# Optimization experiments

Measured on AMD Instinct MI355X. Metric: run time of the kernel, lower is better.

## Reference

```python
import math
import jax, jax.numpy as jnp
import numpy as np

SEQ, BATCH, HID, N_HEAD = 1024, 8, 1024, 16


def setup_inputs() -> dict:
    key0 = jax.random.key(0)
    ks = jax.random.split(key0, 7)
    shp = (SEQ, BATCH, HID)
    w = lambda k: jax.random.normal(k, (HID, HID), dtype=jnp.float32) * 0.02
    return {
        "value": jax.random.normal(ks[0], shp, dtype=jnp.float32),
        "key": jax.random.normal(ks[1], shp, dtype=jnp.float32),
        "query": jax.random.normal(ks[2], shp, dtype=jnp.float32),
        "Wq": w(ks[3]), "Wk": w(ks[4]), "Wv": w(ks[5]), "Wo": w(ks[6]),
    }


def _proj_split(x, W, n_head, d_k):
    # x: (S,B,H) -> linear -> split heads -> stack heads along batch dim: (S, n_head*B, d_k)
    S, B, H = x.shape
    p = x @ W.T                                   # (S,B,H)
    p = p.reshape(S, B, n_head, d_k)
    p = p.transpose(0, 2, 1, 3).reshape(S, n_head * B, d_k)
    return p


def reference(value, key, query, Wq, Wk, Wv, Wo):
    S, B, H = value.shape
    n_head = N_HEAD
    d_k = H // n_head
    Q = _proj_split(query, Wq, n_head, d_k)       # (S, n_head*B, d_k)
    K = _proj_split(key, Wk, n_head, d_k)
    V = _proj_split(value, Wv, n_head, d_k)
    # scores[b,i,j] = K_i . Q_j / sqrt(d_k)  (note: rows = key index, cols = query index)
    scores = jnp.einsum('ibd,jbd->bij', K, Q) / math.sqrt(d_k)  # (n_head*B, S, S)
    future_mask = jnp.triu(jnp.ones((S, S), dtype=bool), 1)      # True where j > i
    scores = jnp.where(future_mask[None, :, :], -jnp.inf, scores)
    # faithful to original: softmax over dim=2 (the QUERY axis)
    dist = jax.nn.softmax(scores, axis=2)                         # (n_head*B, S, S)
    # att[j,b,d] = sum_i dist[b,i,j] * V[i,b,d]
    att = jnp.einsum('bij,ibd->jbd', dist, V)                     # (S, n_head*B, d_k)
    # un-stack heads: (S, n_head, B, d_k) -> (B, S, n_head*d_k)
    att = att.reshape(S, n_head, B, d_k).transpose(2, 0, 1, 3).reshape(B, S, H)
    out = (att @ Wo.T).transpose(1, 0, 2)                         # (S, B, H)
    return out, dist
```

## Files before the change

kernel.cpp:

```cpp
#include <hip/hip_runtime.h>
#include <hip/hip_bf16.h>
#include <stdint.h>

#define SQ   1024
#define NB   8
#define HD   1024
#define NHD  16
#define DKK  64

typedef __bf16 bf16x8_t __attribute__((ext_vector_type(8)));
typedef __bf16 bf16x4_t __attribute__((ext_vector_type(4)));
typedef float  f32x4_t  __attribute__((ext_vector_type(4)));
typedef __hip_bfloat16 bf16;

__device__ __forceinline__ void gld_lds16(const void* g, void* l) {
    __builtin_amdgcn_global_load_lds(
        (__attribute__((address_space(1))) void*)const_cast<void*>(g),
        (__attribute__((address_space(3))) void*)l,
        16, 0, 0);
}

__device__ __forceinline__ bf16x8_t cvt8(float4 a, float4 b) {
    bf16x8_t r;
    r[0] = (__bf16)a.x; r[1] = (__bf16)a.y; r[2] = (__bf16)a.z; r[3] = (__bf16)a.w;
    r[4] = (__bf16)b.x; r[5] = (__bf16)b.y; r[6] = (__bf16)b.z; r[7] = (__bf16)b.w;
    return r;
}

__device__ __forceinline__ void stage64(const char* gbase, int rowstride,
                                        char* lbase, int w, int lane) {
#pragma unroll
    for (int q = 0; q < 2; ++q) {
        const int cid = (q * 4 + w) * 64 + lane;
        const int r   = cid >> 3;
        const int cc  = (cid & 7) ^ ((r ^ (r >> 3)) & 7);
        gld_lds16(gbase + r * rowstride + cc * 16, lbase + cid * 16);
    }
}

__global__ __launch_bounds__(256, 2)
void gemm_kernel(const void* __restrict__ A0, const void* __restrict__ A1,
                 const void* __restrict__ A2,
                 const float* __restrict__ W0, const float* __restrict__ W1,
                 const float* __restrict__ W2,
                 void* __restrict__ O0, void* __restrict__ O1,
                 void* __restrict__ O2, int mode)
{
    const int z = blockIdx.z;
    const void*  A  = (z == 0) ? A0 : (z == 1) ? A1 : A2;
    const float* Wf = (z == 0) ? W0 : (z == 1) ? W1 : W2;
    void*        Ov = (z == 0) ? O0 : (z == 1) ? O1 : O2;

    __shared__ alignas(16) bf16 lA[2][128 * 32];
    __shared__ alignas(16) bf16 lB[2][128 * 32];

    const int tid  = threadIdx.x;
    const int lane = tid & 63;
    const int w    = tid >> 6;
    const int wr   = w >> 1;
    const int wc   = w & 1;
    const int g    = lane >> 4;
    const int ln   = lane & 15;
    const int bm   = blockIdx.y;
    const int bn   = blockIdx.x;

    f32x4_t acc[4][4];
#pragma unroll
    for (int i = 0; i < 4; ++i)
#pragma unroll
        for (int j = 0; j < 4; ++j)
            acc[i][j] = (f32x4_t){0.f, 0.f, 0.f, 0.f};

    const size_t arow0 = (size_t)bm * 128;
    const size_t brow0 = (size_t)bn * 128;
    const float* Af = (const float*)A;
    const bf16*  Ab = (const bf16*)A;

    int scid[2], srow[2], sch[2];
#pragma unroll
    for (int q = 0; q < 2; ++q) {
        const int cid = (q * 4 + w) * 64 + lane;
        scid[q] = cid;
        srow[q] = cid >> 2;
        sch[q]  = (cid & 3) ^ ((srow[q] ^ (srow[q] >> 2)) & 3);
    }

    float4 pa[4], pw[4];

    auto issue_loads = [&](int k0, int buf) {
#pragma unroll
        for (int q = 0; q < 2; ++q) {
            const float4* wsrc = (const float4*)(Wf + (brow0 + srow[q]) * HD + k0 + sch[q] * 8);
            pw[q * 2]     = wsrc[0];
            pw[q * 2 + 1] = wsrc[1];
        }
        if (mode == 0) {
#pragma unroll
            for (int q = 0; q < 2; ++q) {
                const float4* asrc = (const float4*)(Af + (arow0 + srow[q]) * HD + k0 + sch[q] * 8);
                pa[q * 2]     = asrc[0];
                pa[q * 2 + 1] = asrc[1];
            }
        } else {
#pragma unroll
            for (int q = 0; q < 2; ++q)
                gld_lds16((const char*)Ab + ((arow0 + srow[q]) * HD + k0) * 2 + sch[q] * 16,
                          (char*)&lA[buf][0] + scid[q] * 16);
        }
    };
    auto commit_writes = [&](int buf) {
#pragma unroll
        for (int q = 0; q < 2; ++q)
            *(bf16x8_t*)&lB[buf][scid[q] * 8] = cvt8(pw[q * 2], pw[q * 2 + 1]);
        if (mode == 0) {
#pragma unroll
            for (int q = 0; q < 2; ++q)
                *(bf16x8_t*)&lA[buf][scid[q] * 8] = cvt8(pa[q * 2], pa[q * 2 + 1]);
        }
    };

    issue_loads(0, 0);
    commit_writes(0);
    __syncthreads();

    int cur = 0;
    for (int ks = 0; ks < 32; ++ks) {
        if (ks < 31) issue_loads((ks + 1) * 32, cur ^ 1);
        bf16x8_t av[4], bv[4];
#pragma unroll
        for (int mi = 0; mi < 4; ++mi) {
            const int row = wr * 64 + mi * 16 + ln;
            av[mi] = *(const bf16x8_t*)&lA[cur][row * 32 + ((g ^ ((row ^ (row >> 2)) & 3)) << 3)];
        }
#pragma unroll
        for (int ni = 0; ni < 4; ++ni) {
            const int row = wc * 64 + ni * 16 + ln;
            bv[ni] = *(const bf16x8_t*)&lB[cur][row * 32 + ((g ^ ((row ^ (row >> 2)) & 3)) << 3)];
        }
#pragma unroll
        for (int mi = 0; mi < 4; ++mi)
#pragma unroll
            for (int ni = 0; ni < 4; ++ni)
                acc[mi][ni] = __builtin_amdgcn_mfma_f32_16x16x32_bf16(
                    av[mi], bv[ni], acc[mi][ni], 0, 0, 0);
        if (ks < 31) commit_writes(cur ^ 1);
        __syncthreads();
        cur ^= 1;
    }

    bf16*  Ob = (bf16*)Ov;
    float* Of = (float*)Ov;
#pragma unroll
    for (int mi = 0; mi < 4; ++mi) {
#pragma unroll
        for (int ni = 0; ni < 4; ++ni) {
            const int o = bn * 128 + wc * 64 + ni * 16 + ln;
#pragma unroll
            for (int r = 0; r < 4; ++r) {
                const int m = bm * 128 + wr * 64 + mi * 16 + g * 4 + r;
                const float v = acc[mi][ni][r];
                if (mode == 0) {
                    const int h = o >> 6, d = o & 63;
                    const int s = m >> 3, b = m & 7;
                    if (z == 2)
                        Ob[((size_t)((h * 8 + b) * DKK + d)) * SQ + s] = __float2bfloat16(v);
                    else
                        Ob[(((size_t)(h * 8 + b) * SQ + s) << 6) + d] = __float2bfloat16(v);
                } else {
                    Of[(size_t)m * HD + o] = v;
                }
            }
        }
    }
}

__global__ __launch_bounds__(256, 2)
void rowsum_kernel(const bf16* __restrict__ Kh, const bf16* __restrict__ Qh,
                   float* __restrict__ invS)
{
    __shared__ alignas(16) bf16 Kl[64 * 64];
    __shared__ alignas(16) bf16 Ql[2][64 * 64];
    const int tid = threadIdx.x, lane = tid & 63, w = tid >> 6;
    const int g = lane >> 4, ln = lane & 15;
    const int ib = 15 - (int)blockIdx.x, bh = blockIdx.y;
    const char* Kp = (const char*)(Kh + ((size_t)bh * SQ + ib * 64) * DKK);
    const char* Qp = (const char*)(Qh + (size_t)bh * SQ * DKK);

    stage64(Kp, 128, (char*)Kl, w, lane);
    stage64(Qp, 128, (char*)Ql[0], w, lane);
    __syncthreads();

    const int arow = w * 16 + ln;
    const int asw  = (arow ^ (arow >> 3)) & 7;
    const bf16x8_t ak0 = *(const bf16x8_t*)&Kl[arow * 64 + ((g ^ asw) << 3)];
    const bf16x8_t ak1 = *(const bf16x8_t*)&Kl[arow * 64 + (((4 + g) ^ asw) << 3)];
    const int irow = ib * 64 + w * 16 + g * 4;

    float lsum[4] = {0.f, 0.f, 0.f, 0.f};
    int cur = 0;
    for (int jt = 0; jt <= ib; ++jt) {
        if (jt < ib)
            stage64(Qp + (size_t)(jt + 1) * 8192, 128, (char*)Ql[cur ^ 1], w, lane);
#pragma unroll
        for (int nf = 0; nf < 4; ++nf) {
            const int brow = nf * 16 + ln;
            const int bsw  = (brow ^ (brow >> 3)) & 7;
            bf16x8_t b0 = *(const bf16x8_t*)&Ql[cur][brow * 64 + ((g ^ bsw) << 3)];
            bf16x8_t b1 = *(const bf16x8_t*)&Ql[cur][brow * 64 + (((4 + g) ^ bsw) << 3)];
            f32x4_t a = (f32x4_t){0.f, 0.f, 0.f, 0.f};
            __builtin_amdgcn_s_setprio(1);
            a = __builtin_amdgcn_mfma_f32_16x16x32_bf16(ak0, b0, a, 0, 0, 0);
            a = __builtin_amdgcn_mfma_f32_16x16x32_bf16(ak1, b1, a, 0, 0, 0);
            __builtin_amdgcn_s_setprio(0);
            const int j = jt * 64 + nf * 16 + ln;
#pragma unroll
            for (int r = 0; r < 4; ++r)
                lsum[r] += (j <= irow + r) ? __expf(a[r] * 0.125f) : 0.f;
        }
        __syncthreads();
        cur ^= 1;
    }
#pragma unroll
    for (int r = 0; r < 4; ++r) {
        float p = lsum[r];
        p += __shfl_xor(p, 1);
        p += __shfl_xor(p, 2);
        p += __shfl_xor(p, 4);
        p += __shfl_xor(p, 8);
        lsum[r] = p;
    }
    if (ln == 0) {
#pragma unroll
        for (int r = 0; r < 4; ++r)
            invS[(size_t)bh * SQ + irow + r] = 1.f / lsum[r];
    }
}

__global__ __launch_bounds__(256, 2)
void dist_pv_kernel(const bf16* __restrict__ Kh, const bf16* __restrict__ Qh,
                    const bf16* __restrict__ Vt, const float* __restrict__ invS,
                    float* __restrict__ Dist, bf16* __restrict__ att4)
{
    __shared__ alignas(16) bf16 Kl[2][64 * 64];
    __shared__ alignas(16) bf16 Vl[2][64 * 64];
    __shared__ alignas(16) bf16 Ql[64 * 64];
    __shared__ alignas(16) bf16 dT[64 * 72];
    __shared__ alignas(16) float dF[64 * 68];
    const int tid = threadIdx.x, lane = tid & 63, w = tid >> 6;
    const int g = lane >> 4, ln = lane & 15;
    const int jb = blockIdx.x, bh = blockIdx.y;
    const char* Kp = (const char*)(Kh + (size_t)bh * SQ * DKK);
    const char* Qp = (const char*)(Qh + (size_t)bh * SQ * DKK);
    const char* Vp = (const char*)(Vt + (size_t)bh * DKK * SQ);
    float* Dp = Dist + (size_t)bh * SQ * SQ;
    const float* ivp = invS + (size_t)bh * SQ;

    stage64(Qp + (size_t)jb * 8192, 128, (char*)Ql, w, lane);
    __syncthreads();
    bf16x8_t bq[4][2];
#pragma unroll
    for (int nf = 0; nf < 4; ++nf) {
        const int brow = nf * 16 + ln;
        const int bsw  = (brow ^ (brow >> 3)) & 7;
        bq[nf][0] = *(const bf16x8_t*)&Ql[brow * 64 + ((g ^ bsw) << 3)];
        bq[nf][1] = *(const bf16x8_t*)&Ql[brow * 64 + (((4 + g) ^ bsw) << 3)];
    }

    stage64(Kp + (size_t)jb * 8192, 128, (char*)Kl[0], w, lane);
    stage64(Vp + (size_t)jb * 128, 2048, (char*)Vl[0], w, lane);

    const f32x4_t zero4 = (f32x4_t){0.f, 0.f, 0.f, 0.f};
    for (int it0 = 0; it0 < jb; ++it0) {
#pragma unroll
        for (int q = 0; q < 4; ++q) {
            const int cid = q * 256 + tid;
            const int row = cid >> 4, ch = cid & 15;
            *(f32x4_t*)(Dp + (size_t)(it0 * 64 + row) * SQ + jb * 64 + ch * 4) = zero4;
        }
    }
    __syncthreads();

    const int arow = w * 16 + ln;
    const int asw  = (arow ^ (arow >> 3)) & 7;
    f32x4_t accPV[4];
#pragma unroll
    for (int nf = 0; nf < 4; ++nf) accPV[nf] = zero4;

    int cur = 0;
    for (int it = jb; it < 16; ++it) {
        if (it < 15) {
            stage64(Kp + (size_t)(it + 1) * 8192, 128, (char*)Kl[cur ^ 1], w, lane);
            stage64(Vp + (size_t)(it + 1) * 128, 2048, (char*)Vl[cur ^ 1], w, lane);
        }
        const int i0 = it * 64 + w * 16 + g * 4;
        float iv[4];
#pragma unroll
        for (int r = 0; r < 4; ++r) iv[r] = ivp[i0 + r];

        const bf16x8_t ak0 = *(const bf16x8_t*)&Kl[cur][arow * 64 + ((g ^ asw) << 3)];
        const bf16x8_t ak1 = *(const bf16x8_t*)&Kl[cur][arow * 64 + (((4 + g) ^ asw) << 3)];
#pragma unroll
        for (int nf = 0; nf < 4; ++nf) {
            f32x4_t a = zero4;
            __builtin_amdgcn_s_setprio(1);
            a = __builtin_amdgcn_mfma_f32_16x16x32_bf16(ak0, bq[nf][0], a, 0, 0, 0);
            a = __builtin_amdgcn_mfma_f32_16x16x32_bf16(ak1, bq[nf][1], a, 0, 0, 0);
            __builtin_amdgcn_s_setprio(0);
            const int jl = nf * 16 + ln;
            const int j  = jb * 64 + jl;
            bf16x4_t pk;
#pragma unroll
            for (int r = 0; r < 4; ++r) {
                const float e = (j <= i0 + r) ? __expf(a[r] * 0.125f) * iv[r] : 0.f;
                dF[(w * 16 + g * 4 + r) * 68 + jl] = e;
                pk[r] = (__bf16)e;
            }
            *(bf16x4_t*)&dT[jl * 72 + ((w * 16 + g * 4) ^ (((jl >> 3) & 7) << 3))] = pk;
        }
        __syncthreads();

#pragma unroll
        for (int q = 0; q < 4; ++q) {
            const int cid = q * 256 + tid;
            const int row = cid >> 4;
            const int jc  = (cid & 15) << 2;
            const f32x4_t fv = *(const f32x4_t*)&dF[row * 68 + jc];
            *(f32x4_t*)(Dp + (size_t)(it * 64 + row) * SQ + jb * 64 + jc) = fv;
        }
#pragma unroll
        for (int kk = 0; kk < 2; ++kk) {
            const int abase = (kk * 32 + g * 8) ^ (((arow >> 3) & 7) << 3);
            const bf16x8_t a = *(const bf16x8_t*)&dT[arow * 72 + abase];
            __builtin_amdgcn_s_setprio(1);
#pragma unroll
            for (int nf = 0; nf < 4; ++nf) {
                const int brow = nf * 16 + ln;
                const int bsw  = (brow ^ (brow >> 3)) & 7;
                const bf16x8_t b =
                    *(const bf16x8_t*)&Vl[cur][brow * 64 + (((kk * 4 + g) ^ bsw) << 3)];
                accPV[nf] = __builtin_amdgcn_mfma_f32_16x16x32_bf16(a, b, accPV[nf], 0, 0, 0);
            }
            __builtin_amdgcn_s_setprio(0);
        }
        __syncthreads();
        cur ^= 1;
    }

    const int h = bh >> 3, b = bh & 7;
#pragma unroll
    for (int nf = 0; nf < 4; ++nf) {
#pragma unroll
        for (int r = 0; r < 4; ++r) {
            const int j = jb * 64 + w * 16 + g * 4 + r;
            att4[(size_t)(j * 8 + b) * HD + h * 64 + nf * 16 + ln] =
                __float2bfloat16(accPV[nf][r]);
        }
    }
}

extern "C" void kernel_launch(void* const* d_in, const int* in_sizes, int n_in,
                              void* d_out, int out_size, void* d_ws, size_t ws_size,
                              hipStream_t stream)
{
    const float* value = (const float*)d_in[0];
    const float* key_  = (const float*)d_in[1];
    const float* query = (const float*)d_in[2];
    const float* Wq    = (const float*)d_in[3];
    const float* Wk    = (const float*)d_in[4];
    const float* Wv    = (const float*)d_in[5];
    const float* Wo    = (const float*)d_in[6];

    float* out  = (float*)d_out;
    float* dist = out + (size_t)SQ * NB * HD;
    float* invS = out;

    char* ws   = (char*)d_ws;
    bf16* Qh   = (bf16*)(ws);
    bf16* Kh   = (bf16*)(ws + (size_t)16 * 1024 * 1024);
    bf16* Vt   = (bf16*)(ws + (size_t)32 * 1024 * 1024);
    bf16* att4 = (bf16*)(ws + (size_t)48 * 1024 * 1024);

    dim3 blk(256);
    gemm_kernel<<<dim3(8, 64, 3), blk, 0, stream>>>(
        query, key_, value, Wq, Wk, Wv, Qh, Kh, Vt, 0);
    rowsum_kernel<<<dim3(16, 128), blk, 0, stream>>>(Kh, Qh, invS);
    dist_pv_kernel<<<dim3(16, 128), blk, 0, stream>>>(Kh, Qh, Vt, invS, dist, att4);
    gemm_kernel<<<dim3(8, 64, 1), blk, 0, stream>>>(
        att4, att4, att4, Wo, Wo, Wo, out, out, out, 1);
}
```

Measured before the change: 940.8 us.

## Pre-convert inputs to bf16, triple-buffer projection GEMM, restructure dist/PV pipeline

Adds a separate conversion pass that turns the fp32 activations and weights into bf16 scratch held in the dist output region, so the QKV projection GEMM can stage both operands through direct global-to-LDS loads with a 3-stage buffer and explicit vmcnt waits. Upper-triangle zeroing of dist moves from the dist/PV kernel into the rowsum kernel. The dist/PV kernel drops its fp32 LDS staging tile and writes probabilities straight to global, and uses double-buffered dT with lighter barriers. Occupancy hints are raised. The trade is an extra conversion pass over the inputs in exchange for less in-loop conversion and fewer barriers, at the risk of less coalesced dist stores.

```diff
diff --git a/kernel.cpp b/kernel.cpp
--- a/kernel.cpp
+++ b/kernel.cpp
@@ -13,6 +13,8 @@
 typedef float  f32x4_t  __attribute__((ext_vector_type(4)));
 typedef __hip_bfloat16 bf16;
 
+#define SB0() __builtin_amdgcn_sched_barrier(0)
+
 __device__ __forceinline__ void gld_lds16(const void* g, void* l) {
     __builtin_amdgcn_global_load_lds(
         (__attribute__((address_space(1))) void*)const_cast<void*>(g),
@@ -20,6 +22,19 @@
         16, 0, 0);
 }
 
+__device__ __forceinline__ void vm_bar() {
+    SB0();
+    asm volatile("s_waitcnt vmcnt(0) lgkmcnt(0)" ::: "memory");
+    __builtin_amdgcn_s_barrier();
+    SB0();
+}
+__device__ __forceinline__ void lgkm_bar() {
+    SB0();
+    asm volatile("s_waitcnt lgkmcnt(0)" ::: "memory");
+    __builtin_amdgcn_s_barrier();
+    SB0();
+}
+
 __device__ __forceinline__ bf16x8_t cvt8(float4 a, float4 b) {
     bf16x8_t r;
     r[0] = (__bf16)a.x; r[1] = (__bf16)a.y; r[2] = (__bf16)a.z; r[3] = (__bf16)a.w;
@@ -38,21 +53,47 @@
     }
 }
 
-__global__ __launch_bounds__(256, 2)
-void gemm_kernel(const void* __restrict__ A0, const void* __restrict__ A1,
-                 const void* __restrict__ A2,
-                 const float* __restrict__ W0, const float* __restrict__ W1,
-                 const float* __restrict__ W2,
-                 void* __restrict__ O0, void* __restrict__ O1,
-                 void* __restrict__ O2, int mode)
+__device__ __forceinline__ void stage_g(const char* gbase, char* lbase,
+                                        int w, int lane) {
+#pragma unroll
+    for (int q = 0; q < 2; ++q) {
+        const int cid = (q * 4 + w) * 64 + lane;
+        const int r   = cid >> 2;
+        const int ch  = (cid & 3) ^ ((r ^ (r >> 2)) & 3);
+        gld_lds16(gbase + r * (HD * 2) + ch * 16, lbase + cid * 16);
+    }
+}
+
+__global__ __launch_bounds__(256)
+void cvt_kernel(const float* __restrict__ s0, const float* __restrict__ s1,
+                const float* __restrict__ s2,
+                bf16* __restrict__ d0, bf16* __restrict__ d1,
+                bf16* __restrict__ d2)
 {
     const int z = blockIdx.z;
-    const void*  A  = (z == 0) ? A0 : (z == 1) ? A1 : A2;
-    const float* Wf = (z == 0) ? W0 : (z == 1) ? W1 : W2;
-    void*        Ov = (z == 0) ? O0 : (z == 1) ? O1 : O2;
-
-    __shared__ alignas(16) bf16 lA[2][128 * 32];
-    __shared__ alignas(16) bf16 lB[2][128 * 32];
+    const float* s = (z == 0) ? s0 : (z == 1) ? s1 : s2;
+    bf16*        d = (z == 0) ? d0 : (z == 1) ? d1 : d2;
+    const size_t i = ((size_t)blockIdx.x * 256 + threadIdx.x) * 8;
+    const float4 a = *(const float4*)(s + i);
+    const float4 b = *(const float4*)(s + i + 4);
+    *(bf16x8_t*)(d + i) = cvt8(a, b);
+}
+
+__global__ __launch_bounds__(256, 3)
+void gemm_bb(const bf16* __restrict__ A0, const bf16* __restrict__ A1,
+             const bf16* __restrict__ A2,
+             const bf16* __restrict__ B0, const bf16* __restrict__ B1,
+             const bf16* __restrict__ B2,
+             bf16* __restrict__ O0, bf16* __restrict__ O1,
+             bf16* __restrict__ O2)
+{
+    const int z = blockIdx.z;
+    const bf16* A  = (z == 0) ? A0 : (z == 1) ? A1 : A2;
+    const bf16* Bw = (z == 0) ? B0 : (z == 1) ? B1 : B2;
+    bf16*       Ob = (z == 0) ? O0 : (z == 1) ? O1 : O2;
+
+    __shared__ alignas(16) bf16 lA[3][128 * 32];
+    __shared__ alignas(16) bf16 lB[3][128 * 32];
 
     const int tid  = threadIdx.x;
     const int lane = tid & 63;
@@ -71,10 +112,93 @@
         for (int j = 0; j < 4; ++j)
             acc[i][j] = (f32x4_t){0.f, 0.f, 0.f, 0.f};
 
+    const char* Ap = (const char*)(A  + (size_t)bm * 128 * HD);
+    const char* Bp = (const char*)(Bw + (size_t)bn * 128 * HD);
+
+    auto stg = [&](int ks, int buf) {
+        stage_g(Ap + ks * 64, (char*)&lA[buf][0], w, lane);
+        stage_g(Bp + ks * 64, (char*)&lB[buf][0], w, lane);
+    };
+
+    stg(0, 0);
+    stg(1, 1);
+
+    for (int ks = 0; ks < 32; ++ks) {
+        const int buf = ks % 3;
+        SB0();
+        if (ks < 31) asm volatile("s_waitcnt vmcnt(4)" ::: "memory");
+        else         asm volatile("s_waitcnt vmcnt(0)" ::: "memory");
+        __builtin_amdgcn_s_barrier();
+        SB0();
+        if (ks < 30) stg(ks + 2, (ks + 2) % 3);
+
+        bf16x8_t av[4], bv[4];
+#pragma unroll
+        for (int mi = 0; mi < 4; ++mi) {
+            const int row = wr * 64 + mi * 16 + ln;
+            av[mi] = *(const bf16x8_t*)&lA[buf][row * 32 + ((g ^ ((row ^ (row >> 2)) & 3)) << 3)];
+        }
+#pragma unroll
+        for (int ni = 0; ni < 4; ++ni) {
+            const int row = wc * 64 + ni * 16 + ln;
+            bv[ni] = *(const bf16x8_t*)&lB[buf][row * 32 + ((g ^ ((row ^ (row >> 2)) & 3)) << 3)];
+        }
+        __builtin_amdgcn_s_setprio(1);
+#pragma unroll
+        for (int mi = 0; mi < 4; ++mi)
+#pragma unroll
+            for (int ni = 0; ni < 4; ++ni)
+                acc[mi][ni] = __builtin_amdgcn_mfma_f32_16x16x32_bf16(
+                    av[mi], bv[ni], acc[mi][ni], 0, 0, 0);
+        __builtin_amdgcn_s_setprio(0);
+    }
+
+#pragma unroll
+    for (int mi = 0; mi < 4; ++mi) {
+#pragma unroll
+        for (int ni = 0; ni < 4; ++ni) {
+            const int o = bn * 128 + wc * 64 + ni * 16 + ln;
+#pragma unroll
+            for (int r = 0; r < 4; ++r) {
+                const int m = bm * 128 + wr * 64 + mi * 16 + g * 4 + r;
+                const float v = acc[mi][ni][r];
+                const int h = o >> 6, d = o & 63;
+                const int s = m >> 3, b = m & 7;
+                if (z == 2)
+                    Ob[((size_t)((h * 8 + b) * DKK + d)) * SQ + s] = __float2bfloat16(v);
+                else
+                    Ob[(((size_t)(h * 8 + b) * SQ + s) << 6) + d] = __float2bfloat16(v);
+            }
+        }
+    }
+}
+
+__global__ __launch_bounds__(256, 2)
+void gemm_k4(const bf16* __restrict__ A, const float* __restrict__ Wf,
+             float* __restrict__ Of)
+{
+    __shared__ alignas(16) bf16 lA[2][128 * 32];
+    __shared__ alignas(16) bf16 lB[2][128 * 32];
+
+    const int tid  = threadIdx.x;
+    const int lane = tid & 63;
+    const int w    = tid >> 6;
+    const int wr   = w >> 1;
+    const int wc   = w & 1;
+    const int g    = lane >> 4;
+    const int ln   = lane & 15;
+    const int bm   = blockIdx.y;
+    const int bn   = blockIdx.x;
+
+    f32x4_t acc[4][4];
+#pragma unroll
+    for (int i = 0; i < 4; ++i)
+#pragma unroll
+        for (int j = 0; j < 4; ++j)
+            acc[i][j] = (f32x4_t){0.f, 0.f, 0.f, 0.f};
+
     const size_t arow0 = (size_t)bm * 128;
     const size_t brow0 = (size_t)bn * 128;
-    const float* Af = (const float*)A;
-    const bf16*  Ab = (const bf16*)A;
 
     int scid[2], srow[2], sch[2];
 #pragma unroll
@@ -85,7 +209,7 @@
         sch[q]  = (cid & 3) ^ ((srow[q] ^ (srow[q] >> 2)) & 3);
     }
 
-    float4 pa[4], pw[4];
+    float4 pw[4];
 
     auto issue_loads = [&](int k0, int buf) {
 #pragma unroll
@@ -94,29 +218,15 @@
             pw[q * 2]     = wsrc[0];
             pw[q * 2 + 1] = wsrc[1];
         }
-        if (mode == 0) {
-#pragma unroll
-            for (int q = 0; q < 2; ++q) {
-                const float4* asrc = (const float4*)(Af + (arow0 + srow[q]) * HD + k0 + sch[q] * 8);
-                pa[q * 2]     = asrc[0];
-                pa[q * 2 + 1] = asrc[1];
-            }
-        } else {
-#pragma unroll
-            for (int q = 0; q < 2; ++q)
-                gld_lds16((const char*)Ab + ((arow0 + srow[q]) * HD + k0) * 2 + sch[q] * 16,
-                          (char*)&lA[buf][0] + scid[q] * 16);
-        }
+#pragma unroll
+        for (int q = 0; q < 2; ++q)
+            gld_lds16((const char*)A + ((arow0 + srow[q]) * HD + k0) * 2 + sch[q] * 16,
+                      (char*)&lA[buf][0] + scid[q] * 16);
     };
     auto commit_writes = [&](int buf) {
 #pragma unroll
         for (int q = 0; q < 2; ++q)
             *(bf16x8_t*)&lB[buf][scid[q] * 8] = cvt8(pw[q * 2], pw[q * 2 + 1]);
-        if (mode == 0) {
-#pragma unroll
-            for (int q = 0; q < 2; ++q)
-                *(bf16x8_t*)&lA[buf][scid[q] * 8] = cvt8(pa[q * 2], pa[q * 2 + 1]);
-        }
     };
 
     issue_loads(0, 0);
@@ -148,8 +258,6 @@
         cur ^= 1;
     }
 
-    bf16*  Ob = (bf16*)Ov;
-    float* Of = (float*)Ov;
 #pragma unroll
     for (int mi = 0; mi < 4; ++mi) {
 #pragma unroll
@@ -158,25 +266,15 @@
 #pragma unroll
             for (int r = 0; r < 4; ++r) {
                 const int m = bm * 128 + wr * 64 + mi * 16 + g * 4 + r;
-                const float v = acc[mi][ni][r];
-                if (mode == 0) {
-                    const int h = o >> 6, d = o & 63;
-                    const int s = m >> 3, b = m & 7;
-                    if (z == 2)
-                        Ob[((size_t)((h * 8 + b) * DKK + d)) * SQ + s] = __float2bfloat16(v);
-                    else
-                        Ob[(((size_t)(h * 8 + b) * SQ + s) << 6) + d] = __float2bfloat16(v);
-                } else {
-                    Of[(size_t)m * HD + o] = v;
-                }
+                Of[(size_t)m * HD + o] = acc[mi][ni][r];
             }
         }
     }
 }
 
-__global__ __launch_bounds__(256, 2)
+__global__ __launch_bounds__(256, 4)
 void rowsum_kernel(const bf16* __restrict__ Kh, const bf16* __restrict__ Qh,
-                   float* __restrict__ invS)
+                   float* __restrict__ invS, float* __restrict__ Dist)
 {
     __shared__ alignas(16) bf16 Kl[64 * 64];
     __shared__ alignas(16) bf16 Ql[2][64 * 64];
@@ -185,10 +283,11 @@
     const int ib = 15 - (int)blockIdx.x, bh = blockIdx.y;
     const char* Kp = (const char*)(Kh + ((size_t)bh * SQ + ib * 64) * DKK);
     const char* Qp = (const char*)(Qh + (size_t)bh * SQ * DKK);
+    float* Dp = Dist + (size_t)bh * SQ * SQ;
 
     stage64(Kp, 128, (char*)Kl, w, lane);
     stage64(Qp, 128, (char*)Ql[0], w, lane);
-    __syncthreads();
+    vm_bar();
 
     const int arow = w * 16 + ln;
     const int asw  = (arow ^ (arow >> 3)) & 7;
@@ -197,16 +296,17 @@
     const int irow = ib * 64 + w * 16 + g * 4;
 
     float lsum[4] = {0.f, 0.f, 0.f, 0.f};
-    int cur = 0;
     for (int jt = 0; jt <= ib; ++jt) {
+        const int buf = jt & 1;
+        if (jt > 0) vm_bar();
         if (jt < ib)
-            stage64(Qp + (size_t)(jt + 1) * 8192, 128, (char*)Ql[cur ^ 1], w, lane);
+            stage64(Qp + (size_t)(jt + 1) * 8192, 128, (char*)Ql[buf ^ 1], w, lane);
 #pragma unroll
         for (int nf = 0; nf < 4; ++nf) {
             const int brow = nf * 16 + ln;
             const int bsw  = (brow ^ (brow >> 3)) & 7;
-            bf16x8_t b0 = *(const bf16x8_t*)&Ql[cur][brow * 64 + ((g ^ bsw) << 3)];
-            bf16x8_t b1 = *(const bf16x8_t*)&Ql[cur][brow * 64 + (((4 + g) ^ bsw) << 3)];
+            bf16x8_t b0 = *(const bf16x8_t*)&Ql[buf][brow * 64 + ((g ^ bsw) << 3)];
+            bf16x8_t b1 = *(const bf16x8_t*)&Ql[buf][brow * 64 + (((4 + g) ^ bsw) << 3)];
             f32x4_t a = (f32x4_t){0.f, 0.f, 0.f, 0.f};
             __builtin_amdgcn_s_setprio(1);
             a = __builtin_amdgcn_mfma_f32_16x16x32_bf16(ak0, b0, a, 0, 0, 0);
@@ -217,8 +317,6 @@
             for (int r = 0; r < 4; ++r)
                 lsum[r] += (j <= irow + r) ? __expf(a[r] * 0.125f) : 0.f;
         }
-        __syncthreads();
-        cur ^= 1;
     }
 #pragma unroll
     for (int r = 0; r < 4; ++r) {
@@ -234,18 +332,25 @@
         for (int r = 0; r < 4; ++r)
             invS[(size_t)bh * SQ + irow + r] = 1.f / lsum[r];
     }
-}
-
-__global__ __launch_bounds__(256, 2)
+    const f32x4_t zero4 = (f32x4_t){0.f, 0.f, 0.f, 0.f};
+    for (int jt = ib + 1; jt < 16; ++jt) {
+#pragma unroll
+        for (int q = 0; q < 4; ++q) {
+            const int cid = q * 256 + tid;
+            const int row = cid >> 4, ch = cid & 15;
+            *(f32x4_t*)(Dp + (size_t)(ib * 64 + row) * SQ + jt * 64 + ch * 4) = zero4;
+        }
+    }
+}
+
+__global__ __launch_bounds__(256, 3)
 void dist_pv_kernel(const bf16* __restrict__ Kh, const bf16* __restrict__ Qh,
                     const bf16* __restrict__ Vt, const float* __restrict__ invS,
                     float* __restrict__ Dist, bf16* __restrict__ att4)
 {
     __shared__ alignas(16) bf16 Kl[2][64 * 64];
     __shared__ alignas(16) bf16 Vl[2][64 * 64];
-    __shared__ alignas(16) bf16 Ql[64 * 64];
-    __shared__ alignas(16) bf16 dT[64 * 72];
-    __shared__ alignas(16) float dF[64 * 68];
+    __shared__ alignas(16) bf16 dT[2][64 * 72];
     const int tid = threadIdx.x, lane = tid & 63, w = tid >> 6;
     const int g = lane >> 4, ln = lane & 15;
     const int jb = blockIdx.x, bh = blockIdx.y;
@@ -255,53 +360,46 @@
     float* Dp = Dist + (size_t)bh * SQ * SQ;
     const float* ivp = invS + (size_t)bh * SQ;
 
-    stage64(Qp + (size_t)jb * 8192, 128, (char*)Ql, w, lane);
-    __syncthreads();
+    stage64(Qp + (size_t)jb * 8192, 128, (char*)&dT[0][0], w, lane);
+    stage64(Kp + (size_t)jb * 8192, 128, (char*)&Kl[0][0], w, lane);
+    stage64(Vp + (size_t)jb * 128, 2048, (char*)&Vl[0][0], w, lane);
+    vm_bar();
+
     bf16x8_t bq[4][2];
-#pragma unroll
-    for (int nf = 0; nf < 4; ++nf) {
-        const int brow = nf * 16 + ln;
-        const int bsw  = (brow ^ (brow >> 3)) & 7;
-        bq[nf][0] = *(const bf16x8_t*)&Ql[brow * 64 + ((g ^ bsw) << 3)];
-        bq[nf][1] = *(const bf16x8_t*)&Ql[brow * 64 + (((4 + g) ^ bsw) << 3)];
-    }
-
-    stage64(Kp + (size_t)jb * 8192, 128, (char*)Kl[0], w, lane);
-    stage64(Vp + (size_t)jb * 128, 2048, (char*)Vl[0], w, lane);
-
-    const f32x4_t zero4 = (f32x4_t){0.f, 0.f, 0.f, 0.f};
-    for (int it0 = 0; it0 < jb; ++it0) {
-#pragma unroll
-        for (int q = 0; q < 4; ++q) {
-            const int cid = q * 256 + tid;
-            const int row = cid >> 4, ch = cid & 15;
-            *(f32x4_t*)(Dp + (size_t)(it0 * 64 + row) * SQ + jb * 64 + ch * 4) = zero4;
-        }
-    }
-    __syncthreads();
+    {
+        const bf16* Qlp = &dT[0][0];
+#pragma unroll
+        for (int nf = 0; nf < 4; ++nf) {
+            const int brow = nf * 16 + ln;
+            const int bsw  = (brow ^ (brow >> 3)) & 7;
+            bq[nf][0] = *(const bf16x8_t*)&Qlp[brow * 64 + ((g ^ bsw) << 3)];
+            bq[nf][1] = *(const bf16x8_t*)&Qlp[brow * 64 + (((4 + g) ^ bsw) << 3)];
+        }
+    }
 
     const int arow = w * 16 + ln;
     const int asw  = (arow ^ (arow >> 3)) & 7;
     f32x4_t accPV[4];
 #pragma unroll
-    for (int nf = 0; nf < 4; ++nf) accPV[nf] = zero4;
-
-    int cur = 0;
+    for (int nf = 0; nf < 4; ++nf) accPV[nf] = (f32x4_t){0.f, 0.f, 0.f, 0.f};
+
     for (int it = jb; it < 16; ++it) {
+        const int cb = (it - jb) & 1;
+        vm_bar();
         if (it < 15) {
-            stage64(Kp + (size_t)(it + 1) * 8192, 128, (char*)Kl[cur ^ 1], w, lane);
-            stage64(Vp + (size_t)(it + 1) * 128, 2048, (char*)Vl[cur ^ 1], w, lane);
+            stage64(Kp + (size_t)(it + 1) * 8192, 128, (char*)&Kl[cb ^ 1][0], w, lane);
+            stage64(Vp + (size_t)(it + 1) * 128, 2048, (char*)&Vl[cb ^ 1][0], w, lane);
         }
         const int i0 = it * 64 + w * 16 + g * 4;
         float iv[4];
 #pragma unroll
         for (int r = 0; r < 4; ++r) iv[r] = ivp[i0 + r];
 
-        const bf16x8_t ak0 = *(const bf16x8_t*)&Kl[cur][arow * 64 + ((g ^ asw) << 3)];
-        const bf16x8_t ak1 = *(const bf16x8_t*)&Kl[cur][arow * 64 + (((4 + g) ^ asw) << 3)];
+        const bf16x8_t ak0 = *(const bf16x8_t*)&Kl[cb][arow * 64 + ((g ^ asw) << 3)];
+        const bf16x8_t ak1 = *(const bf16x8_t*)&Kl[cb][arow * 64 + (((4 + g) ^ asw) << 3)];
 #pragma unroll
         for (int nf = 0; nf < 4; ++nf) {
-            f32x4_t a = zero4;
+            f32x4_t a = (f32x4_t){0.f, 0.f, 0.f, 0.f};
             __builtin_amdgcn_s_setprio(1);
             a = __builtin_amdgcn_mfma_f32_16x16x32_bf16(ak0, bq[nf][0], a, 0, 0, 0);
             a = __builtin_amdgcn_mfma_f32_16x16x32_bf16(ak1, bq[nf][1], a, 0, 0, 0);
@@ -312,38 +410,27 @@
 #pragma unroll
             for (int r = 0; r < 4; ++r) {
                 const float e = (j <= i0 + r) ? __expf(a[r] * 0.125f) * iv[r] : 0.f;
-                dF[(w * 16 + g * 4 + r) * 68 + jl] = e;
+                Dp[(size_t)(i0 + r) * SQ + j] = e;
                 pk[r] = (__bf16)e;
             }
-            *(bf16x4_t*)&dT[jl * 72 + ((w * 16 + g * 4) ^ (((jl >> 3) & 7) << 3))] = pk;
-        }
-        __syncthreads();
-
-#pragma unroll
-        for (int q = 0; q < 4; ++q) {
-            const int cid = q * 256 + tid;
-            const int row = cid >> 4;
-            const int jc  = (cid & 15) << 2;
-            const f32x4_t fv = *(const f32x4_t*)&dF[row * 68 + jc];
-            *(f32x4_t*)(Dp + (size_t)(it * 64 + row) * SQ + jb * 64 + jc) = fv;
-        }
+            *(bf16x4_t*)&dT[cb][jl * 72 + ((w * 16 + g * 4) ^ (((jl >> 3) & 7) << 3))] = pk;
+        }
+        lgkm_bar();
 #pragma unroll
         for (int kk = 0; kk < 2; ++kk) {
             const int abase = (kk * 32 + g * 8) ^ (((arow >> 3) & 7) << 3);
-            const bf16x8_t a = *(const bf16x8_t*)&dT[arow * 72 + abase];
+            const bf16x8_t a = *(const bf16x8_t*)&dT[cb][arow * 72 + abase];
             __builtin_amdgcn_s_setprio(1);
 #pragma unroll
             for (int nf = 0; nf < 4; ++nf) {
                 const int brow = nf * 16 + ln;
                 const int bsw  = (brow ^ (brow >> 3)) & 7;
                 const bf16x8_t b =
-                    *(const bf16x8_t*)&Vl[cur][brow * 64 + (((kk * 4 + g) ^ bsw) << 3)];
+                    *(const bf16x8_t*)&Vl[cb][brow * 64 + (((kk * 4 + g) ^ bsw) << 3)];
                 accPV[nf] = __builtin_amdgcn_mfma_f32_16x16x32_bf16(a, b, accPV[nf], 0, 0, 0);
             }
             __builtin_amdgcn_s_setprio(0);
         }
-        __syncthreads();
-        cur ^= 1;
     }
 
     const int h = bh >> 3, b = bh & 7;
@@ -374,6 +461,13 @@
     float* dist = out + (size_t)SQ * NB * HD;
     float* invS = out;
 
+    bf16* qb  = (bf16*)dist;
+    bf16* kb  = qb  + (size_t)SQ * NB * HD;
+    bf16* vb  = kb  + (size_t)SQ * NB * HD;
+    bf16* wqb = vb  + (size_t)SQ * NB * HD;
+    bf16* wkb = wqb + (size_t)HD * HD;
+    bf16* wvb = wkb + (size_t)HD * HD;
+
     char* ws   = (char*)d_ws;
     bf16* Qh   = (bf16*)(ws);
     bf16* Kh   = (bf16*)(ws + (size_t)16 * 1024 * 1024);
@@ -381,10 +475,11 @@
     bf16* att4 = (bf16*)(ws + (size_t)48 * 1024 * 1024);
 
     dim3 blk(256);
-    gemm_kernel<<<dim3(8, 64, 3), blk, 0, stream>>>(
-        query, key_, value, Wq, Wk, Wv, Qh, Kh, Vt, 0);
-    rowsum_kernel<<<dim3(16, 128), blk, 0, stream>>>(Kh, Qh, invS);
+    cvt_kernel<<<dim3(4096, 1, 3), blk, 0, stream>>>(query, key_, value, qb, kb, vb);
+    cvt_kernel<<<dim3(512, 1, 3), blk, 0, stream>>>(Wq, Wk, Wv, wqb, wkb, wvb);
+    gemm_bb<<<dim3(8, 64, 3), blk, 0, stream>>>(
+        qb, kb, vb, wqb, wkb, wvb, Qh, Kh, Vt);
+    rowsum_kernel<<<dim3(16, 128), blk, 0, stream>>>(Kh, Qh, invS, dist);
     dist_pv_kernel<<<dim3(16, 128), blk, 0, stream>>>(Kh, Qh, Vt, invS, dist, att4);
-    gemm_kernel<<<dim3(8, 64, 1), blk, 0, stream>>>(
-        att4, att4, att4, Wo, Wo, Wo, out, out, out, 1);
-}
+    gemm_k4<<<dim3(8, 64), blk, 0, stream>>>(att4, Wo, out);
+}
```

New measurement: 903.0 us. 4.0% less time.
